# Kernel tuning notes

Measured on AMD Instinct MI355X. Metric: run time of the kernel, lower is better.

Reference implementation:

```python
import jax, jax.numpy as jnp
import numpy as np

ROPE_THETA = 10000.0
NH, D_NOPE, D_ROPE, D_V = 16, 128, 64, 128
D_QK = D_NOPE + D_ROPE  # 192
KV_LORA = 512
SCALING = D_QK ** -0.5
EPS = 1e-6


def rmsnorm(x, w):
    xf = x.astype(jnp.float32)
    var = jnp.mean(xf * xf, axis=-1, keepdims=True)
    return (w * (xf * jax.lax.rsqrt(var + EPS))).astype(x.dtype)


def rotate_half(x):
    x1, x2 = jnp.split(x, 2, axis=-1)
    return jnp.concatenate([-x2, x1], axis=-1)


def rope_cos_sin(seq_len, dim, dtype):
    inv_freq = 1.0 / (ROPE_THETA ** (jnp.arange(0, dim, 2, dtype=jnp.float32) / dim))
    t = jnp.arange(seq_len, dtype=jnp.float32)
    ang = jnp.outer(t, inv_freq)              # [S, dim/2]
    emb = jnp.concatenate([ang, ang], axis=-1)  # [S, dim]
    return jnp.cos(emb).astype(dtype), jnp.sin(emb).astype(dtype)


def setup_inputs() -> dict:
    key = jax.random.key(0)
    ks = jax.random.split(key, 8)
    B, S, H, QLR = 2, 2048, 2048, 1536
    s = lambda k, shape, fan: jax.random.normal(k, shape, jnp.float32) * (fan ** -0.5)
    return {
        "hidden_states": jax.random.normal(ks[0], (B, S, H), jnp.float32),
        "q_a_w": s(ks[1], (QLR, H), H),
        "q_a_ln_w": jnp.ones((QLR,), jnp.float32),
        "q_b_w": s(ks[2], (NH * D_QK, QLR), QLR),
        "kv_a_w": s(ks[3], (KV_LORA + D_ROPE, H), H),
        "kv_a_ln_w": jnp.ones((KV_LORA,), jnp.float32),
        "kv_b_w": s(ks[4], (NH * (D_NOPE + D_V), KV_LORA), KV_LORA),
        "o_w": s(ks[5], (H, NH * D_V), NH * D_V),
    }


def reference(hidden_states, q_a_w, q_a_ln_w, q_b_w, kv_a_w, kv_a_ln_w, kv_b_w, o_w):
    B, S, H = hidden_states.shape
    # --- Q path: low-rank compression -> norm -> up-proj ---
    q_a = hidden_states @ q_a_w.T                         # [B,S,QLR]
    q = rmsnorm(q_a, q_a_ln_w) @ q_b_w.T                  # [B,S,NH*D_QK]
    q = q.reshape(B, S, NH, D_QK).transpose(0, 2, 1, 3)   # [B,NH,S,D_QK]
    q_nope, q_rope = q[..., :D_NOPE], q[..., D_NOPE:]
    # --- KV path: joint compression with MQA rope branch ---
    kv_a = hidden_states @ kv_a_w.T                       # [B,S,KV_LORA+D_ROPE]
    c_kv, k_rope = kv_a[..., :KV_LORA], kv_a[..., KV_LORA:]
    kv = rmsnorm(c_kv, kv_a_ln_w) @ kv_b_w.T              # [B,S,NH*(D_NOPE+D_V)]
    kv = kv.reshape(B, S, NH, D_NOPE + D_V).transpose(0, 2, 1, 3)
    k_nope, v = kv[..., :D_NOPE], kv[..., D_NOPE:]        # [B,NH,S,*]
    k_rope = k_rope[:, None, :, :]                        # [B,1,S,D_ROPE] shared across heads
    # --- decoupled RoPE on rope sub-dims only ---
    cos, sin = rope_cos_sin(S, D_ROPE, hidden_states.dtype)
    q_rope = q_rope * cos + rotate_half(q_rope) * sin
    k_rope = k_rope * cos + rotate_half(k_rope) * sin
    k_rope = jnp.broadcast_to(k_rope, (B, NH, S, D_ROPE))
    q_full = jnp.concatenate([q_nope, q_rope], axis=-1)   # [B,NH,S,D_QK]
    k_full = jnp.concatenate([k_nope, k_rope], axis=-1)
    # --- causal attention ---
    scores = jnp.einsum("bhqd,bhkd->bhqk", q_full, k_full) * SCALING
    causal = jnp.tril(jnp.ones((S, S), bool))
    scores = jnp.where(causal, scores, jnp.finfo(scores.dtype).min)
    attn = jax.nn.softmax(scores.astype(jnp.float32), axis=-1).astype(v.dtype)
    out = jnp.einsum("bhqk,bhkd->bhqd", attn, v)          # [B,NH,S,D_V]
    out = out.transpose(0, 2, 1, 3).reshape(B, S, NH * D_V)
    return out @ o_w.T                                    # [B,S,H]
```

## Files before the change

### kernel.cpp

```cpp
#include <hip/hip_runtime.h>
#include <hip/hip_bf16.h>
#include <math.h>
#include <stdint.h>

#define NHEADS 16
#define DQK 192
#define DVDIM 128
#define SEQ 2048
#define BATCH 2
#define MROWS 4096
#define HDIM 2048
#define QLORA 1536
#define KVLORA 512
#define SCALING 0.07216878364870323f
#define NTQ 32

typedef __attribute__((ext_vector_type(8))) short short8;
typedef __attribute__((ext_vector_type(4))) short short4v;
typedef __attribute__((ext_vector_type(4))) float f32x4;

__device__ __forceinline__ float4 ld4(const float* p) {
    return *reinterpret_cast<const float4*>(p);
}
__device__ __forceinline__ unsigned short f2b(float x) {
    __hip_bfloat16 h = __float2bfloat16(x);
    return __builtin_bit_cast(unsigned short, h);
}
__device__ __forceinline__ void gload16(const void* g, void* l) {
    typedef const __attribute__((address_space(1))) unsigned int ga_t;
    typedef __attribute__((address_space(3))) unsigned int ls_t;
    __builtin_amdgcn_global_load_lds((ga_t*)(uintptr_t)g, (ls_t*)(uintptr_t)l, 16, 0, 0);
}

__global__ __launch_bounds__(256) void cvt_bf(const float* __restrict__ in,
                                              unsigned short* __restrict__ o, int n8) {
    int i = blockIdx.x * 256 + threadIdx.x;
    if (i >= n8) return;
    float4 a = ld4(in + (size_t)i * 8), b = ld4(in + (size_t)i * 8 + 4);
    short8 t;
    t[0] = (short)f2b(a.x); t[1] = (short)f2b(a.y); t[2] = (short)f2b(a.z); t[3] = (short)f2b(a.w);
    t[4] = (short)f2b(b.x); t[5] = (short)f2b(b.y); t[6] = (short)f2b(b.z); t[7] = (short)f2b(b.w);
    *(short8*)(o + (size_t)i * 8) = t;
}

template <int MODE>
__global__ __launch_bounds__(256) void gemm_bf16(
        const unsigned short* __restrict__ A, int lda,
        const unsigned short* __restrict__ W, const unsigned short* __restrict__ W2,
        float* __restrict__ Cf, int ldc,
        unsigned short* __restrict__ O1, unsigned short* __restrict__ O2,
        const float* __restrict__ cosb, const float* __restrict__ sinb,
        int K) {
    __shared__ unsigned short As[2][128 * 32];
    __shared__ unsigned short Bs[2][128 * 32];

    const int tid = threadIdx.x;
    const int bm = blockIdx.y * 128, bn = blockIdx.x * 128;
    const int w = tid >> 6, lane = tid & 63;
    const int wr = (w >> 1) * 64, wc = (w & 1) * 64;
    const int fr = lane & 15, fq = lane >> 4;

    const int r0 = w * 32 + (lane >> 2);
    const int c0 = (lane & 3) * 8;

    const unsigned short* Ag0;
    if constexpr (MODE == 4) {
        Ag0 = A + (size_t)((bm >> 7) * 256 + 128 + r0) * lda + c0;
    } else {
        Ag0 = A + (size_t)(bm + r0) * lda + c0;
    }
    const unsigned short* Ag1 = Ag0 + (size_t)16 * lda;

    const unsigned short* Wg0;
    const unsigned short* Wg1;
    if constexpr (MODE == 1) {
        if (bn < 1536) {
            Wg0 = W + (size_t)(bn + r0) * K + c0;
            Wg1 = Wg0 + (size_t)16 * K;
        } else {
            int br0 = bn - 1536 + r0;      if (br0 > 575) br0 = 575;
            int br1 = bn - 1536 + r0 + 16; if (br1 > 575) br1 = 575;
            Wg0 = W2 + (size_t)br0 * K + c0;
            Wg1 = W2 + (size_t)br1 * K + c0;
        }
    } else if constexpr (MODE == 3) {
        Wg0 = W + (size_t)((bn >> 7) * 256 + r0) * K + c0;
        Wg1 = Wg0 + (size_t)16 * K;
    } else {
        Wg0 = W + (size_t)(bn + r0) * K + c0;
        Wg1 = Wg0 + (size_t)16 * K;
    }

#define STAGE(buf, koff) do { \
        gload16(Ag0 + (koff), &As[buf][(w * 32) * 32]); \
        gload16(Ag1 + (koff), &As[buf][(w * 32 + 16) * 32]); \
        gload16(Wg0 + (koff), &Bs[buf][(w * 32) * 32]); \
        gload16(Wg1 + (koff), &Bs[buf][(w * 32 + 16) * 32]); \
    } while (0)

    f32x4 acc[4][4];
    #pragma unroll
    for (int m = 0; m < 4; m++)
        #pragma unroll
        for (int n = 0; n < 4; n++) acc[m][n] = (f32x4)0.0f;

    const int NT = K >> 5;
    STAGE(0, 0);
    __syncthreads();
    int cur = 0;
    for (int t = 0; t < NT; t++) {
        const int kn = (t + 1 < NT) ? (t + 1) * 32 : 0;
        STAGE(cur ^ 1, kn);

        short8 af[4], bfr[4];
        #pragma unroll
        for (int m = 0; m < 4; m++)
            af[m] = *(const short8*)&As[cur][(wr + m * 16 + fr) * 32 + fq * 8];
        #pragma unroll
        for (int n = 0; n < 4; n++)
            bfr[n] = *(const short8*)&Bs[cur][(wc + n * 16 + fr) * 32 + fq * 8];
        #pragma unroll
        for (int m = 0; m < 4; m++)
            #pragma unroll
            for (int n = 0; n < 4; n++)
                acc[m][n] = __builtin_amdgcn_mfma_f32_16x16x32_bf16(af[m], bfr[n], acc[m][n], 0, 0, 0);

        __syncthreads();
        cur ^= 1;
    }
#undef STAGE

    if constexpr (MODE == 0) {
        #pragma unroll
        for (int m = 0; m < 4; m++)
            #pragma unroll
            for (int n = 0; n < 4; n++) {
                const int col = bn + wc + n * 16 + fr;
                #pragma unroll
                for (int j = 0; j < 4; j++)
                    Cf[(size_t)(bm + wr + m * 16 + fq * 4 + j) * ldc + col] = acc[m][n][j];
            }
    } else if constexpr (MODE == 1) {
        #pragma unroll
        for (int m = 0; m < 4; m++)
            #pragma unroll
            for (int n = 0; n < 4; n++) {
                const int col = bn + wc + n * 16 + fr;
                if (col < 2112) {
                    #pragma unroll
                    for (int j = 0; j < 4; j++)
                        Cf[(size_t)(bm + wr + m * 16 + fq * 4 + j) * 2112 + col] = acc[m][n][j];
                }
            }
    } else if constexpr (MODE == 2) {
        #pragma unroll
        for (int n = 0; n < 4; n++) {
            const int col = bn + wc + n * 16 + fr;
            const int h = col / DQK, d = col % DQK;
            #pragma unroll
            for (int m = 0; m < 4; m++) {
                #pragma unroll
                for (int j = 0; j < 4; j++) {
                    const int row = bm + wr + m * 16 + fq * 4 + j;
                    const int s = row & (SEQ - 1), b = row >> 11;
                    float v = acc[m][n][j];
                    if (d >= DVDIM) {
                        const int j5 = d - DVDIM;
                        const float partner = acc[m][n ^ 2][j];
                        const float rot = (j5 < 32) ? -partner : partner;
                        v = v * cosb[s * 64 + j5] + rot * sinb[s * 64 + j5];
                    }
                    O1[((size_t)(b * NHEADS + h) * SEQ + s) * DQK + d] = f2b(v);
                }
            }
        }
    } else if constexpr (MODE == 3) {
        #pragma unroll
        for (int n = 0; n < 4; n++) {
            const int col = bn + wc + n * 16 + fr;
            const int h = col >> 7, d = col & 127;
            #pragma unroll
            for (int m = 0; m < 4; m++) {
                #pragma unroll
                for (int j = 0; j < 4; j++) {
                    const int row = bm + wr + m * 16 + fq * 4 + j;
                    const int s = row & (SEQ - 1);
                    const int bh = (row >> 11) * NHEADS + h;
                    O1[((size_t)bh * SEQ + s) * DQK + d] = f2b(acc[m][n][j]);
                }
            }
        }
    } else {
        #pragma unroll
        for (int n = 0; n < 4; n++) {
            const int col = bn + wc + n * 16 + fr;
            const int b = col >> 11, s = col & (SEQ - 1);
            #pragma unroll
            for (int m = 0; m < 4; m++) {
                #pragma unroll
                for (int j = 0; j < 4; j++) {
                    const int vf = bm + wr + m * 16 + fq * 4 + j;
                    const int h = vf >> 7, dv = vf & 127;
                    O2[((size_t)(b * NHEADS + h) * DVDIM + dv) * SEQ + s] = f2b(acc[m][n][j]);
                }
            }
        }
    }
}

__global__ __launch_bounds__(256) void rmsnorm_bf(const float* __restrict__ x,
                                                  const float* __restrict__ w,
                                                  unsigned short* __restrict__ o,
                                                  int ncols, int instride) {
    const float* xr = x + (size_t)blockIdx.x * instride;
    unsigned short* orow = o + (size_t)blockIdx.x * ncols;
    const int tid = threadIdx.x;
    float ss = 0.f;
    for (int c = tid * 4; c < ncols; c += 1024) {
        float4 v = ld4(xr + c);
        ss += v.x * v.x + v.y * v.y + v.z * v.z + v.w * v.w;
    }
    #pragma unroll
    for (int d = 32; d > 0; d >>= 1) ss += __shfl_down(ss, d);
    __shared__ float wsum[4];
    if ((tid & 63) == 0) wsum[tid >> 6] = ss;
    __syncthreads();
    float total = wsum[0] + wsum[1] + wsum[2] + wsum[3];
    float scale = 1.0f / sqrtf(total / (float)ncols + 1e-6f);
    for (int c = tid * 4; c < ncols; c += 1024) {
        float4 v = ld4(xr + c);
        short4v t;
        t[0] = (short)f2b(v.x * scale * w[c + 0]);
        t[1] = (short)f2b(v.y * scale * w[c + 1]);
        t[2] = (short)f2b(v.z * scale * w[c + 2]);
        t[3] = (short)f2b(v.w * scale * w[c + 3]);
        *(short4v*)&orow[c] = t;
    }
}

__global__ void rope_table(float* __restrict__ cost, float* __restrict__ sint) {
    int s = blockIdx.x, j = threadIdx.x;
    int i = j & 31;
    float inv = 1.0f / powf(10000.0f, (float)i * (1.0f / 32.0f));
    float ang = (float)s * inv;
    cost[s * 64 + j] = cosf(ang);
    sint[s * 64 + j] = sinf(ang);
}

__global__ void rope_k_bcast(const float* __restrict__ qkva,
                             const float* __restrict__ cost,
                             const float* __restrict__ sint,
                             unsigned short* __restrict__ kbf) {
    const int r = blockIdx.x;
    const int j = threadIdx.x;
    const int b = r >> 11, s = r & (SEQ - 1);
    const float* base = qkva + (size_t)r * 2112 + 2048;
    const float x = base[j];
    const float rot = (j < 32) ? -base[j + 32] : base[j - 32];
    const unsigned short v = f2b(x * cost[s * 64 + j] + rot * sint[s * 64 + j]);
    #pragma unroll
    for (int h = 0; h < NHEADS; h++)
        kbf[((size_t)(b * NHEADS + h) * SEQ + s) * DQK + DVDIM + j] = v;
}

__global__ __launch_bounds__(256, 2) void flash_mfma(const unsigned short* __restrict__ qbf,
                                                     const unsigned short* __restrict__ kbf,
                                                     const unsigned short* __restrict__ vbfT,
                                                     unsigned short* __restrict__ attn) {
    __shared__ unsigned short Ks[64][200];
    __shared__ unsigned short Vs[128][72];
    __shared__ unsigned short Ps[4][16][72];

    const int lin = blockIdx.x;
    const int xcd = lin & 7;
    const int idx = lin >> 3;
    const int bh = xcd * 4 + (idx >> 4);
    const int bx = idx & 15;
    const int b = bh >> 4, h = bh & 15;
    const int tid = threadIdx.x;
    const int w = tid >> 6, lane = tid & 63;
    const int fr = lane & 15, fq = lane >> 4;

    const unsigned short* Qh = qbf + ((size_t)bh * SEQ) * DQK;
    const unsigned short* Kh = kbf + ((size_t)bh * SEQ) * DQK;
    const unsigned short* Vh = vbfT + ((size_t)bh * 128) * SEQ;

    short8 kreg[6], vreg[4];
    #pragma unroll
    for (int u = 0; u < 6; u++) {
        int i = tid + u * 256;
        int row = i / 24, c = (i % 24) * 8;
        kreg[u] = *(const short8*)(Kh + (size_t)row * DQK + c);
    }
    #pragma unroll
    for (int u = 0; u < 4; u++) {
        int i = tid + u * 256;
        int row = i >> 3, c = (i & 7) * 8;
        vreg[u] = *(const short8*)(Vh + (size_t)row * SEQ + c);
    }

    #pragma unroll 1
    for (int pass = 0; pass < 2; pass++) {
        const int qt = pass ? (NTQ - 1 - bx) : bx;
        const int q0 = qt * 64;

        short8 qf[6];
        {
            const unsigned short* qrow = Qh + (size_t)(q0 + w * 16 + fr) * DQK;
            #pragma unroll
            for (int kw = 0; kw < 6; kw++)
                qf[kw] = *(const short8*)(qrow + kw * 32 + fq * 8);
        }

        f32x4 acc[8];
        #pragma unroll
        for (int n = 0; n < 8; n++) acc[n] = (f32x4)0.0f;
        float mrow[4], lrow[4];
        #pragma unroll
        for (int j = 0; j < 4; j++) { mrow[j] = -3.0e38f; lrow[j] = 0.0f; }

        #pragma unroll 1
        for (int t = 0; t <= qt; t++) {
            __syncthreads();
            #pragma unroll
            for (int u = 0; u < 6; u++) {
                int i = tid + u * 256;
                int row = i / 24, c = (i % 24) * 8;
                *(short8*)&Ks[row][c] = kreg[u];
            }
            #pragma unroll
            for (int u = 0; u < 4; u++) {
                int i = tid + u * 256;
                int row = i >> 3, c = (i & 7) * 8;
                *(short8*)&Vs[row][c] = vreg[u];
            }
            __syncthreads();

            const int nt = (t < qt) ? (t + 1) : (pass == 0 ? 0 : -1);
            if (nt >= 0) {
                const int kt0n = nt * 64;
                #pragma unroll
                for (int u = 0; u < 6; u++) {
                    int i = tid + u * 256;
                    int row = i / 24, c = (i % 24) * 8;
                    kreg[u] = *(const short8*)(Kh + (size_t)(kt0n + row) * DQK + c);
                }
                #pragma unroll
                for (int u = 0; u < 4; u++) {
                    int i = tid + u * 256;
                    int row = i >> 3, c = (i & 7) * 8;
                    vreg[u] = *(const short8*)(Vh + (size_t)row * SEQ + kt0n + c);
                }
            }

            f32x4 sfr[4];
            #pragma unroll
            for (int n = 0; n < 4; n++) sfr[n] = (f32x4)0.0f;
            __builtin_amdgcn_s_setprio(1);
            #pragma unroll
            for (int kw = 0; kw < 6; kw++) {
                #pragma unroll
                for (int n = 0; n < 4; n++) {
                    short8 kf = *(const short8*)&Ks[n * 16 + fr][kw * 32 + fq * 8];
                    sfr[n] = __builtin_amdgcn_mfma_f32_16x16x32_bf16(qf[kw], kf, sfr[n], 0, 0, 0);
                }
            }
            __builtin_amdgcn_s_setprio(0);

            const bool diag = (t == qt);
            float pv[4][4];
            float mnew[4];
            #pragma unroll
            for (int j = 0; j < 4; j++) mnew[j] = mrow[j];
            #pragma unroll
            for (int n = 0; n < 4; n++) {
                #pragma unroll
                for (int j = 0; j < 4; j++) {
                    float s = sfr[n][j] * SCALING;
                    if (diag && (n * 16 + fr > w * 16 + fq * 4 + j)) s = -3.0e38f;
                    pv[n][j] = s;
                    mnew[j] = fmaxf(mnew[j], s);
                }
            }
            #pragma unroll
            for (int j = 0; j < 4; j++) {
                mnew[j] = fmaxf(mnew[j], __shfl_xor(mnew[j], 1));
                mnew[j] = fmaxf(mnew[j], __shfl_xor(mnew[j], 2));
                mnew[j] = fmaxf(mnew[j], __shfl_xor(mnew[j], 4));
                mnew[j] = fmaxf(mnew[j], __shfl_xor(mnew[j], 8));
            }
            float es[4], psum[4];
            #pragma unroll
            for (int j = 0; j < 4; j++) {
                es[j] = __expf(mrow[j] - mnew[j]);
                psum[j] = 0.0f;
            }
            #pragma unroll
            for (int n = 0; n < 4; n++) {
                #pragma unroll
                for (int j = 0; j < 4; j++) {
                    float p = __expf(pv[n][j] - mnew[j]);
                    pv[n][j] = p;
                    psum[j] += p;
                }
            }
            #pragma unroll
            for (int j = 0; j < 4; j++) {
                psum[j] += __shfl_xor(psum[j], 1);
                psum[j] += __shfl_xor(psum[j], 2);
                psum[j] += __shfl_xor(psum[j], 4);
                psum[j] += __shfl_xor(psum[j], 8);
                lrow[j] = lrow[j] * es[j] + psum[j];
                mrow[j] = mnew[j];
            }
            #pragma unroll
            for (int n = 0; n < 8; n++) {
                #pragma unroll
                for (int j = 0; j < 4; j++) acc[n][j] *= es[j];
            }
            #pragma unroll
            for (int n = 0; n < 4; n++) {
                #pragma unroll
                for (int j = 0; j < 4; j++)
                    Ps[w][fq * 4 + j][n * 16 + fr] = f2b(pv[n][j]);
            }
            __builtin_amdgcn_s_setprio(1);
            #pragma unroll
            for (int tt = 0; tt < 2; tt++) {
                short8 pa = *(const short8*)&Ps[w][fr][tt * 32 + fq * 8];
                #pragma unroll
                for (int n = 0; n < 8; n++) {
                    short8 vf = *(const short8*)&Vs[n * 16 + fr][tt * 32 + fq * 8];
                    acc[n] = __builtin_amdgcn_mfma_f32_16x16x32_bf16(pa, vf, acc[n], 0, 0, 0);
                }
            }
            __builtin_amdgcn_s_setprio(0);
        }

        #pragma unroll
        for (int j = 0; j < 4; j++) {
            const float inv = 1.0f / lrow[j];
            unsigned short* orow = attn + (size_t)(b * SEQ + q0 + w * 16 + fq * 4 + j) * (NHEADS * DVDIM) + h * DVDIM;
            #pragma unroll
            for (int n = 0; n < 8; n++)
                orow[n * 16 + fr] = f2b(acc[n][j] * inv);
        }
    }
}

extern "C" void kernel_launch(void* const* d_in, const int* in_sizes, int n_in,
                              void* d_out, int out_size, void* d_ws, size_t ws_size,
                              hipStream_t stream) {
    const float* hidden   = (const float*)d_in[0];
    const float* q_a_w    = (const float*)d_in[1];
    const float* q_a_ln_w = (const float*)d_in[2];
    const float* q_b_w    = (const float*)d_in[3];
    const float* kv_a_w   = (const float*)d_in[4];
    const float* kv_a_ln_w= (const float*)d_in[5];
    const float* kv_b_w   = (const float*)d_in[6];
    const float* o_w      = (const float*)d_in[7];
    float* out = (float*)d_out;

    char* base = (char*)d_ws;
    size_t off = 0;
    auto alloc = [&](size_t bytes) -> void* {
        void* p = base + off;
        off += (bytes + 255) & ~(size_t)255;
        return p;
    };
    float* qkva          = (float*)alloc((size_t)MROWS * 2112 * 4);
    float* cosb          = (float*)alloc((size_t)SEQ * 64 * 4);
    float* sinb          = (float*)alloc((size_t)SEQ * 64 * 4);
    unsigned short* hbf  = (unsigned short*)alloc((size_t)MROWS * HDIM * 2);
    unsigned short* w_qa = (unsigned short*)alloc((size_t)QLORA * HDIM * 2);
    unsigned short* w_qb = (unsigned short*)alloc((size_t)3072 * QLORA * 2);
    unsigned short* w_kva= (unsigned short*)alloc((size_t)576 * HDIM * 2);
    unsigned short* w_kvb= (unsigned short*)alloc((size_t)4096 * KVLORA * 2);
    unsigned short* w_o  = (unsigned short*)alloc((size_t)HDIM * 2048 * 2);
    unsigned short* qabf = (unsigned short*)alloc((size_t)MROWS * QLORA * 2);
    unsigned short* ckvbf= (unsigned short*)alloc((size_t)MROWS * KVLORA * 2);
    unsigned short* qbf  = (unsigned short*)alloc((size_t)32 * SEQ * DQK * 2);
    unsigned short* kbf  = (unsigned short*)alloc((size_t)32 * SEQ * DQK * 2);
    unsigned short* vbfT = (unsigned short*)alloc((size_t)32 * DVDIM * SEQ * 2);
    unsigned short* attnbf=(unsigned short*)alloc((size_t)MROWS * 2048 * 2);

    cvt_bf<<<4096, 256, 0, stream>>>(hidden, hbf, 1048576);
    cvt_bf<<<1536, 256, 0, stream>>>(q_a_w,  w_qa, 393216);
    cvt_bf<<<2304, 256, 0, stream>>>(q_b_w,  w_qb, 589824);
    cvt_bf<<< 576, 256, 0, stream>>>(kv_a_w, w_kva, 147456);
    cvt_bf<<<1024, 256, 0, stream>>>(kv_b_w, w_kvb, 262144);
    cvt_bf<<<2048, 256, 0, stream>>>(o_w,    w_o,  524288);
    rope_table<<<SEQ, 64, 0, stream>>>(cosb, sinb);

    gemm_bf16<1><<<dim3(17, 32), 256, 0, stream>>>(hbf, HDIM, w_qa, w_kva,
                                                   qkva, 2112, nullptr, nullptr,
                                                   nullptr, nullptr, HDIM);
    rmsnorm_bf<<<MROWS, 256, 0, stream>>>(qkva, q_a_ln_w, qabf, QLORA, 2112);
    rmsnorm_bf<<<MROWS, 256, 0, stream>>>(qkva + 1536, kv_a_ln_w, ckvbf, KVLORA, 2112);
    gemm_bf16<2><<<dim3(24, 32), 256, 0, stream>>>(qabf, QLORA, w_qb, nullptr,
                                                   nullptr, 0, qbf, nullptr,
                                                   cosb, sinb, QLORA);
    gemm_bf16<3><<<dim3(16, 32), 256, 0, stream>>>(ckvbf, KVLORA, w_kvb, nullptr,
                                                   nullptr, 0, kbf, nullptr,
                                                   nullptr, nullptr, KVLORA);
    gemm_bf16<4><<<dim3(32, 16), 256, 0, stream>>>(w_kvb, KVLORA, ckvbf, nullptr,
                                                   nullptr, 0, nullptr, vbfT,
                                                   nullptr, nullptr, KVLORA);
    rope_k_bcast<<<MROWS, 64, 0, stream>>>(qkva, cosb, sinb, kbf);
    flash_mfma<<<512, 256, 0, stream>>>(qbf, kbf, vbfT, attnbf);
    gemm_bf16<0><<<dim3(16, 32), 256, 0, stream>>>(attnbf, 2048, w_o, nullptr,
                                                   out, 2048, nullptr, nullptr,
                                                   nullptr, nullptr, 2048);
}
```

Before: 502.9 us.

## Triple-buffer GEMM LDS pipeline and defer softmax rescaling in attention

The GEMM main loop moves from double to triple buffering of the A/B tiles. It keeps two tiles of loads in flight, uses explicit vmcnt waits and a single barrier per iteration, and drops the trailing __syncthreads. Separately, the flash-attention softmax now skips updating the running max (and rescaling the accumulator) when the new tile max exceeds the old by at most 8. The rescale loop is branched on a wave-wide __any. This reduces sync and ALU overhead but uses more LDS per block, and lets exponentials reach up to e^8 before rescaling.

```diff
diff --git a/kernel.cpp b/kernel.cpp
--- a/kernel.cpp
+++ b/kernel.cpp
@@ -51,8 +51,8 @@
         unsigned short* __restrict__ O1, unsigned short* __restrict__ O2,
         const float* __restrict__ cosb, const float* __restrict__ sinb,
         int K) {
-    __shared__ unsigned short As[2][128 * 32];
-    __shared__ unsigned short Bs[2][128 * 32];
+    __shared__ unsigned short As[3][128 * 32];
+    __shared__ unsigned short Bs[3][128 * 32];
 
     const int tid = threadIdx.x;
     const int bm = blockIdx.y * 128, bn = blockIdx.x * 128;
@@ -106,27 +106,33 @@
 
     const int NT = K >> 5;
     STAGE(0, 0);
-    __syncthreads();
-    int cur = 0;
+    STAGE(1, 32);
+    int cb = 0;
     for (int t = 0; t < NT; t++) {
-        const int kn = (t + 1 < NT) ? (t + 1) * 32 : 0;
-        STAGE(cur ^ 1, kn);
+        if (t == NT - 1) asm volatile("s_waitcnt vmcnt(0)" ::: "memory");
+        else             asm volatile("s_waitcnt vmcnt(4)" ::: "memory");
+        __builtin_amdgcn_s_barrier();
+        __builtin_amdgcn_sched_barrier(0);
+
+        if (t + 2 < NT) {
+            int nb = cb + 2; if (nb >= 3) nb -= 3;
+            STAGE(nb, (t + 2) * 32);
+        }
 
         short8 af[4], bfr[4];
         #pragma unroll
         for (int m = 0; m < 4; m++)
-            af[m] = *(const short8*)&As[cur][(wr + m * 16 + fr) * 32 + fq * 8];
+            af[m] = *(const short8*)&As[cb][(wr + m * 16 + fr) * 32 + fq * 8];
         #pragma unroll
         for (int n = 0; n < 4; n++)
-            bfr[n] = *(const short8*)&Bs[cur][(wc + n * 16 + fr) * 32 + fq * 8];
+            bfr[n] = *(const short8*)&Bs[cb][(wc + n * 16 + fr) * 32 + fq * 8];
         #pragma unroll
         for (int m = 0; m < 4; m++)
             #pragma unroll
             for (int n = 0; n < 4; n++)
                 acc[m][n] = __builtin_amdgcn_mfma_f32_16x16x32_bf16(af[m], bfr[n], acc[m][n], 0, 0, 0);
 
-        __syncthreads();
-        cur ^= 1;
+        cb++; if (cb >= 3) cb = 0;
     }
 #undef STAGE
 
@@ -369,9 +375,9 @@
 
             const bool diag = (t == qt);
             float pv[4][4];
-            float mnew[4];
-            #pragma unroll
-            for (int j = 0; j < 4; j++) mnew[j] = mrow[j];
+            float tmax[4];
+            #pragma unroll
+            for (int j = 0; j < 4; j++) tmax[j] = -3.0e38f;
             #pragma unroll
             for (int n = 0; n < 4; n++) {
                 #pragma unroll
@@ -379,20 +385,23 @@
                     float s = sfr[n][j] * SCALING;
                     if (diag && (n * 16 + fr > w * 16 + fq * 4 + j)) s = -3.0e38f;
                     pv[n][j] = s;
-                    mnew[j] = fmaxf(mnew[j], s);
+                    tmax[j] = fmaxf(tmax[j], s);
                 }
             }
             #pragma unroll
             for (int j = 0; j < 4; j++) {
-                mnew[j] = fmaxf(mnew[j], __shfl_xor(mnew[j], 1));
-                mnew[j] = fmaxf(mnew[j], __shfl_xor(mnew[j], 2));
-                mnew[j] = fmaxf(mnew[j], __shfl_xor(mnew[j], 4));
-                mnew[j] = fmaxf(mnew[j], __shfl_xor(mnew[j], 8));
-            }
-            float es[4], psum[4];
+                tmax[j] = fmaxf(tmax[j], __shfl_xor(tmax[j], 1));
+                tmax[j] = fmaxf(tmax[j], __shfl_xor(tmax[j], 2));
+                tmax[j] = fmaxf(tmax[j], __shfl_xor(tmax[j], 4));
+                tmax[j] = fmaxf(tmax[j], __shfl_xor(tmax[j], 8));
+            }
+            bool defer[4];
+            float mnew[4], es[4], psum[4];
             #pragma unroll
             for (int j = 0; j < 4; j++) {
-                es[j] = __expf(mrow[j] - mnew[j]);
+                defer[j] = (tmax[j] - mrow[j] <= 8.0f);
+                mnew[j] = defer[j] ? mrow[j] : tmax[j];
+                es[j] = defer[j] ? 1.0f : __expf(mrow[j] - mnew[j]);
                 psum[j] = 0.0f;
             }
             #pragma unroll
@@ -413,10 +422,13 @@
                 lrow[j] = lrow[j] * es[j] + psum[j];
                 mrow[j] = mnew[j];
             }
-            #pragma unroll
-            for (int n = 0; n < 8; n++) {
-                #pragma unroll
-                for (int j = 0; j < 4; j++) acc[n][j] *= es[j];
+            const bool needresc = !(defer[0] && defer[1] && defer[2] && defer[3]);
+            if (__any(needresc)) {
+                #pragma unroll
+                for (int n = 0; n < 8; n++) {
+                    #pragma unroll
+                    for (int j = 0; j < 4; j++) acc[n][j] *= es[j];
+                }
             }
             #pragma unroll
             for (int n = 0; n < 4; n++) {
```

After: 488.3 us. 1.03x faster.
